# Kernel tuning notes

Measured on AMD Instinct MI355X. Metric: run time of the kernel, lower is better.

The kernel has to match this reference:

```python
import jax, jax.numpy as jnp
import numpy as np

BATCH = 131072
NUM_OSC = 4
NUM_SPEC = 300
FREQ_LO, FREQ_HI = 0.5, 5.0


def setup_inputs() -> dict:
    key = jax.random.key(0)
    ks = jax.random.split(key, 8)
    return {
        "G": jax.random.normal(ks[0], (BATCH, 8), dtype=jnp.float32),
        "W1": jax.random.normal(ks[1], (100, 8), dtype=jnp.float32) * 0.3,
        "b1": jax.random.normal(ks[2], (100,), dtype=jnp.float32) * 0.1,
        "W2": jax.random.normal(ks[3], (100, 100), dtype=jnp.float32) * 0.1,
        "b2": jax.random.normal(ks[4], (100,), dtype=jnp.float32) * 0.1,
        "W_w0": jax.random.normal(ks[5], (NUM_OSC, 100), dtype=jnp.float32) * 0.1,
        "W_wp": jax.random.normal(ks[6], (NUM_OSC, 100), dtype=jnp.float32) * 0.1,
        # torch.nn.init.uniform_(lin_g.weight, a=0.0, b=0.1)
        "W_g": jax.random.uniform(ks[7], (NUM_OSC, 100), dtype=jnp.float32) * 0.1,
    }


def reference(G, W1, b1, W2, b2, W_w0, W_wp, W_g):
    # MLP trunk: 8 -> 100 -> 100, ReLU on both layers
    out = jax.nn.relu(G @ W1.T + b1)
    out = jax.nn.relu(out @ W2.T + b2)          # (B, 100)

    # Oscillator parameter heads (bias-free), ReLU-clamped, shape (B, 4, 1)
    w0 = jax.nn.relu(out @ W_w0.T)[:, :, None]
    wp = jax.nn.relu(out @ W_wp.T)[:, :, None]
    g = jax.nn.relu(out @ W_g.T)[:, :, None]

    # Frequency grid (300,) broadcast against (B, 4, 1)
    w = jnp.arange(FREQ_LO, FREQ_HI, (FREQ_HI - FREQ_LO) / NUM_SPEC, dtype=jnp.float32)

    # Lorentz oscillator imaginary permittivity
    num = (wp ** 2) * (w * g)                   # (B, 4, 300)
    den = (w0 ** 2 - w ** 2) ** 2 + (w ** 2) * (g ** 2)
    e2 = num / den
    return jnp.sum(e2, axis=1)                  # (B, 300)
```

## Files before the change

kernel.cpp:

```cpp
#include <hip/hip_runtime.h>

#define BATCH 131072
#define NS    300
#define H     100
#define BLK   256
#define EPB   128
#define NQ4   (EPB * NS / 4)

#define REP25(M) M(0) M(1) M(2) M(3) M(4) M(5) M(6) M(7) M(8) M(9) M(10) M(11) \
  M(12) M(13) M(14) M(15) M(16) M(17) M(18) M(19) M(20) M(21) M(22) M(23) M(24)

__device__ __forceinline__ float qswap1(float x) {
    return __int_as_float(__builtin_amdgcn_mov_dpp(__float_as_int(x), 0xB1, 0xF, 0xF, true));
}
__device__ __forceinline__ float qswap2(float x) {
    return __int_as_float(__builtin_amdgcn_mov_dpp(__float_as_int(x), 0x4E, 0xF, 0xF, true));
}

__global__ __launch_bounds__(BLK, 2)
void lorentz_fused(const float* __restrict__ G,  const float* __restrict__ W1,
                   const float* __restrict__ b1, const float* __restrict__ W2,
                   const float* __restrict__ b2, const float* __restrict__ Ww0,
                   const float* __restrict__ Wwp, const float* __restrict__ Wg,
                   float* __restrict__ out)
{
    __shared__ float4 sW2c4[H * 4 * 7];
    __shared__ float4 sHead4[H * 4];
    __shared__ float4 sP04[EPB], sP14[EPB], sP24[EPB];
    __shared__ float  sW1[H * 8];
    __shared__ float  sB1[H], sB2[H];

    const int tid = threadIdx.x;

    {
        float* sW2cF = (float*)sW2c4;
        for (int i = tid; i < H * H; i += BLK) {
            int j = i / 100, k = i - j * 100;
            int q = k / 25, kk = k - q * 25;
            sW2cF[(j * 4 + q) * 28 + kk] = W2[i];
        }
        for (int i = tid; i < H * 8; i += BLK) sW1[i] = W1[i];
        for (int i = tid; i < H; i += BLK) { sB1[i] = b1[i]; sB2[i] = b2[i]; }
        float* sHeadF = (float*)sHead4;
        for (int i = tid; i < H * 4; i += BLK) {
            int j = i >> 2, q = i & 3;
            sHeadF[i * 4 + 0] = Ww0[q * H + j];
            sHeadF[i * 4 + 1] = Wwp[q * H + j];
            sHeadF[i * 4 + 2] = Wg [q * H + j];
            sHeadF[i * 4 + 3] = 0.f;
        }
    }
    __syncthreads();

    const int q  = tid & 3;
    const int pr = tid >> 2;
    const int e0 = blockIdx.x * EPB + pr * 2;

    const float4* g0p = (const float4*)(G + (size_t)e0 * 8);
    const float4 ga0 = g0p[0], gb0 = g0p[1];
    const float4 ga1 = g0p[2], gb1 = g0p[3];

#define H1DECL(i) float h1a_##i, h1b_##i;
    REP25(H1DECL)
#undef H1DECL
#define L1(i) { const float4* r = (const float4*)&sW1[(q * 25 + (i)) * 8];       \
        const float4 ra = r[0], rb = r[1];                                       \
        const float bb = sB1[q * 25 + (i)];                                      \
        float s0 = fmaf(ga0.x, ra.x, bb);  float s1 = ga0.y * ra.y;              \
        s0 = fmaf(ga0.z, ra.z, s0);  s1 = fmaf(ga0.w, ra.w, s1);                 \
        s0 = fmaf(gb0.x, rb.x, s0);  s1 = fmaf(gb0.y, rb.y, s1);                 \
        s0 = fmaf(gb0.z, rb.z, s0);  s1 = fmaf(gb0.w, rb.w, s1);                 \
        h1a_##i = fmaxf(s0 + s1, 0.f);                                           \
        float t0 = fmaf(ga1.x, ra.x, bb);  float t1 = ga1.y * ra.y;              \
        t0 = fmaf(ga1.z, ra.z, t0);  t1 = fmaf(ga1.w, ra.w, t1);                 \
        t0 = fmaf(gb1.x, rb.x, t0);  t1 = fmaf(gb1.y, rb.y, t1);                 \
        t0 = fmaf(gb1.z, rb.z, t0);  t1 = fmaf(gb1.w, rb.w, t1);                 \
        h1b_##i = fmaxf(t0 + t1, 0.f); }
    REP25(L1)
#undef L1

    float aw0a = 0.f, awpa = 0.f, agga = 0.f;
    float aw0b = 0.f, awpb = 0.f, aggb = 0.f;

#pragma unroll 2
    for (int j = 0; j < H; ++j) {
        const int cb = (j * 4 + q) * 7;
        const float4 c0 = sW2c4[cb + 0], c1 = sW2c4[cb + 1], c2 = sW2c4[cb + 2],
                     c3 = sW2c4[cb + 3], c4 = sW2c4[cb + 4], c5 = sW2c4[cb + 5],
                     c6 = sW2c4[cb + 6];
        const float4 hv  = sHead4[j * 4 + q];
        const float  b2j = sB2[j];

        float pa = 0.f, pb = 0.f;
#define CH(t, i0, i1, i2, i3)                                                    \
        pa = fmaf(h1a_##i0, c##t.x, pa); pb = fmaf(h1b_##i0, c##t.x, pb);        \
        pa = fmaf(h1a_##i1, c##t.y, pa); pb = fmaf(h1b_##i1, c##t.y, pb);        \
        pa = fmaf(h1a_##i2, c##t.z, pa); pb = fmaf(h1b_##i2, c##t.z, pb);        \
        pa = fmaf(h1a_##i3, c##t.w, pa); pb = fmaf(h1b_##i3, c##t.w, pb);
        CH(0, 0, 1, 2, 3)   CH(1, 4, 5, 6, 7)   CH(2, 8, 9, 10, 11)
        CH(3, 12, 13, 14, 15) CH(4, 16, 17, 18, 19) CH(5, 20, 21, 22, 23)
#undef CH
        pa = fmaf(h1a_24, c6.x, pa); pb = fmaf(h1b_24, c6.x, pb);

        float sa = pa + qswap1(pa); sa += qswap2(sa);
        float sb = pb + qswap1(pb); sb += qswap2(sb);
        const float h2a = fmaxf(sa + b2j, 0.f);
        const float h2b = fmaxf(sb + b2j, 0.f);

        aw0a = fmaf(h2a, hv.x, aw0a); awpa = fmaf(h2a, hv.y, awpa); agga = fmaf(h2a, hv.z, agga);
        aw0b = fmaf(h2b, hv.x, aw0b); awpb = fmaf(h2b, hv.y, awpb); aggb = fmaf(h2b, hv.z, aggb);
    }

    {
        float* P0 = (float*)sP04; float* P1 = (float*)sP14; float* P2 = (float*)sP24;
        const float w0a = fmaxf(aw0a, 0.f), wpa = fmaxf(awpa, 0.f), gga = fmaxf(agga, 0.f);
        const float w0b = fmaxf(aw0b, 0.f), wpb = fmaxf(awpb, 0.f), ggb = fmaxf(aggb, 0.f);
        const int ia = (pr * 2) * 4 + q, ib = (pr * 2 + 1) * 4 + q;
        P0[ia] = w0a * w0a;        P0[ib] = w0b * w0b;
        P1[ia] = gga * gga;        P1[ib] = ggb * ggb;
        P2[ia] = wpa * wpa * gga;  P2[ib] = wpb * wpb * ggb;
    }
    __syncthreads();

    float4* out4 = (float4*)out;
    const size_t base4 = (size_t)blockIdx.x * NQ4;

    for (int it = 0; it < (NQ4 + BLK - 1) / BLK; ++it) {
        const int idx4 = it * BLK + tid;
        if (idx4 < NQ4) {
            const int e  = idx4 / 75;
            const int k4 = idx4 - e * 75;
            const float4 P0 = sP04[e], P1 = sP14[e], P2 = sP24[e];
            const float kb = (float)(k4 << 2);
            float4 r; float* rp = (float*)&r;
#pragma unroll
            for (int i = 0; i < 4; ++i) {
                const float w   = 0.5f + (kb + (float)i) * 0.015f;
                const float wsq = w * w;
                const float t0 = P0.x - wsq, t1 = P0.y - wsq,
                            t2 = P0.z - wsq, t3 = P0.w - wsq;
                const float d0 = fmaf(t0, t0, wsq * P1.x);
                const float d1 = fmaf(t1, t1, wsq * P1.y);
                const float d2 = fmaf(t2, t2, wsq * P1.z);
                const float d3 = fmaf(t3, t3, wsq * P1.w);
                const float d01 = d0 * d1, d23 = d2 * d3;
                const float D   = d01 * d23;
                const float n01 = fmaf(P2.y, d0, P2.x * d1);
                const float n23 = fmaf(P2.w, d2, P2.z * d3);
                const float N   = fmaf(n01, d23, n23 * d01);
                rp[i] = w * (N * __builtin_amdgcn_rcpf(D));
            }
            out4[base4 + idx4] = r;
        }
    }
}

extern "C" void kernel_launch(void* const* d_in, const int* in_sizes, int n_in,
                              void* d_out, int out_size, void* d_ws, size_t ws_size,
                              hipStream_t stream) {
    const float* G   = (const float*)d_in[0];
    const float* W1  = (const float*)d_in[1];
    const float* b1  = (const float*)d_in[2];
    const float* W2  = (const float*)d_in[3];
    const float* b2  = (const float*)d_in[4];
    const float* Ww0 = (const float*)d_in[5];
    const float* Wwp = (const float*)d_in[6];
    const float* Wg  = (const float*)d_in[7];
    float* out = (float*)d_out;

    dim3 grid(BATCH / EPB);
    dim3 block(BLK);
    lorentz_fused<<<grid, block, 0, stream>>>(G, W1, b1, W2, b2, Ww0, Wwp, Wg, out);
}
```

Baseline: 90.90 us.

## Process four batch elements per thread quad to reuse W2 shared-memory loads

Each group of four threads now computes the MLP for four batch elements instead of two, doubling elements per block and halving the grid. Every W2/head value read from shared memory now feeds four FMAs instead of two, cutting LDS traffic and weight staging per element. The cost is roughly double the layer-1 activation registers (100 per thread), which risks spills or lower occupancy under launch_bounds(256,2). Since 256*300/4 divides evenly by the block size, the output loop drops its bounds check.

```diff
diff --git a/kernel.cpp b/kernel.cpp
--- a/kernel.cpp
+++ b/kernel.cpp
@@ -4,7 +4,7 @@
 #define NS    300
 #define H     100
 #define BLK   256
-#define EPB   128
+#define EPB   256
 #define NQ4   (EPB * NS / 4)
 
 #define REP25(M) M(0) M(1) M(2) M(3) M(4) M(5) M(6) M(7) M(8) M(9) M(10) M(11) \
@@ -53,34 +53,36 @@
     __syncthreads();
 
     const int q  = tid & 3;
-    const int pr = tid >> 2;
-    const int e0 = blockIdx.x * EPB + pr * 2;
+    const int gi = tid >> 2;
+    const int e0 = blockIdx.x * EPB + gi * 4;
 
-    const float4* g0p = (const float4*)(G + (size_t)e0 * 8);
-    const float4 ga0 = g0p[0], gb0 = g0p[1];
-    const float4 ga1 = g0p[2], gb1 = g0p[3];
+    const float4* gp = (const float4*)(G + (size_t)e0 * 8);
+    const float4 ga0 = gp[0], gb0 = gp[1];
+    const float4 ga1 = gp[2], gb1 = gp[3];
+    const float4 ga2 = gp[4], gb2 = gp[5];
+    const float4 ga3 = gp[6], gb3 = gp[7];
 
-#define H1DECL(i) float h1a_##i, h1b_##i;
+#define H1DECL(i) float h1a_##i, h1b_##i, h1c_##i, h1d_##i;
     REP25(H1DECL)
 #undef H1DECL
-#define L1(i) { const float4* r = (const float4*)&sW1[(q * 25 + (i)) * 8];       \
-        const float4 ra = r[0], rb = r[1];                                       \
-        const float bb = sB1[q * 25 + (i)];                                      \
-        float s0 = fmaf(ga0.x, ra.x, bb);  float s1 = ga0.y * ra.y;              \
-        s0 = fmaf(ga0.z, ra.z, s0);  s1 = fmaf(ga0.w, ra.w, s1);                 \
-        s0 = fmaf(gb0.x, rb.x, s0);  s1 = fmaf(gb0.y, rb.y, s1);                 \
-        s0 = fmaf(gb0.z, rb.z, s0);  s1 = fmaf(gb0.w, rb.w, s1);                 \
-        h1a_##i = fmaxf(s0 + s1, 0.f);                                           \
-        float t0 = fmaf(ga1.x, ra.x, bb);  float t1 = ga1.y * ra.y;              \
-        t0 = fmaf(ga1.z, ra.z, t0);  t1 = fmaf(ga1.w, ra.w, t1);                 \
-        t0 = fmaf(gb1.x, rb.x, t0);  t1 = fmaf(gb1.y, rb.y, t1);                 \
-        t0 = fmaf(gb1.z, rb.z, t0);  t1 = fmaf(gb1.w, rb.w, t1);                 \
-        h1b_##i = fmaxf(t0 + t1, 0.f); }
+#define L1E(dst, ga, gb)                                                        \
+        { float s0 = fmaf(ga.x, ra.x, bb);  float s1 = ga.y * ra.y;             \
+          s0 = fmaf(ga.z, ra.z, s0);  s1 = fmaf(ga.w, ra.w, s1);                \
+          s0 = fmaf(gb.x, rb.x, s0);  s1 = fmaf(gb.y, rb.y, s1);                \
+          s0 = fmaf(gb.z, rb.z, s0);  s1 = fmaf(gb.w, rb.w, s1);                \
+          dst = fmaxf(s0 + s1, 0.f); }
+#define L1(i) { const float4* r = (const float4*)&sW1[(q * 25 + (i)) * 8];      \
+        const float4 ra = r[0], rb = r[1];                                      \
+        const float bb = sB1[q * 25 + (i)];                                     \
+        L1E(h1a_##i, ga0, gb0)  L1E(h1b_##i, ga1, gb1)                          \
+        L1E(h1c_##i, ga2, gb2)  L1E(h1d_##i, ga3, gb3) }
     REP25(L1)
 #undef L1
 
     float aw0a = 0.f, awpa = 0.f, agga = 0.f;
     float aw0b = 0.f, awpb = 0.f, aggb = 0.f;
+    float aw0c = 0.f, awpc = 0.f, aggc = 0.f;
+    float aw0d = 0.f, awpd = 0.f, aggd = 0.f;
 
 #pragma unroll 2
     for (int j = 0; j < H; ++j) {
@@ -91,67 +93,74 @@
         const float4 hv  = sHead4[j * 4 + q];
         const float  b2j = sB2[j];
 
-        float pa = 0.f, pb = 0.f;
-#define CH(t, i0, i1, i2, i3)                                                    \
-        pa = fmaf(h1a_##i0, c##t.x, pa); pb = fmaf(h1b_##i0, c##t.x, pb);        \
-        pa = fmaf(h1a_##i1, c##t.y, pa); pb = fmaf(h1b_##i1, c##t.y, pb);        \
-        pa = fmaf(h1a_##i2, c##t.z, pa); pb = fmaf(h1b_##i2, c##t.z, pb);        \
-        pa = fmaf(h1a_##i3, c##t.w, pa); pb = fmaf(h1b_##i3, c##t.w, pb);
-        CH(0, 0, 1, 2, 3)   CH(1, 4, 5, 6, 7)   CH(2, 8, 9, 10, 11)
+        float pa = 0.f, pb = 0.f, pc = 0.f, pd = 0.f;
+#define CH1(w, i)                                                               \
+        pa = fmaf(h1a_##i, w, pa); pb = fmaf(h1b_##i, w, pb);                   \
+        pc = fmaf(h1c_##i, w, pc); pd = fmaf(h1d_##i, w, pd);
+#define CH(t, i0, i1, i2, i3)                                                   \
+        CH1(c##t.x, i0) CH1(c##t.y, i1) CH1(c##t.z, i2) CH1(c##t.w, i3)
+        CH(0, 0, 1, 2, 3)     CH(1, 4, 5, 6, 7)     CH(2, 8, 9, 10, 11)
         CH(3, 12, 13, 14, 15) CH(4, 16, 17, 18, 19) CH(5, 20, 21, 22, 23)
+        CH1(c6.x, 24)
 #undef CH
-        pa = fmaf(h1a_24, c6.x, pa); pb = fmaf(h1b_24, c6.x, pb);
-
+#undef CH1
         float sa = pa + qswap1(pa); sa += qswap2(sa);
         float sb = pb + qswap1(pb); sb += qswap2(sb);
+        float sc = pc + qswap1(pc); sc += qswap2(sc);
+        float sd = pd + qswap1(pd); sd += qswap2(sd);
         const float h2a = fmaxf(sa + b2j, 0.f);
         const float h2b = fmaxf(sb + b2j, 0.f);
+        const float h2c = fmaxf(sc + b2j, 0.f);
+        const float h2d = fmaxf(sd + b2j, 0.f);
 
         aw0a = fmaf(h2a, hv.x, aw0a); awpa = fmaf(h2a, hv.y, awpa); agga = fmaf(h2a, hv.z, agga);
         aw0b = fmaf(h2b, hv.x, aw0b); awpb = fmaf(h2b, hv.y, awpb); aggb = fmaf(h2b, hv.z, aggb);
+        aw0c = fmaf(h2c, hv.x, aw0c); awpc = fmaf(h2c, hv.y, awpc); aggc = fmaf(h2c, hv.z, aggc);
+        aw0d = fmaf(h2d, hv.x, aw0d); awpd = fmaf(h2d, hv.y, awpd); aggd = fmaf(h2d, hv.z, aggd);
     }
 
     {
         float* P0 = (float*)sP04; float* P1 = (float*)sP14; float* P2 = (float*)sP24;
-        const float w0a = fmaxf(aw0a, 0.f), wpa = fmaxf(awpa, 0.f), gga = fmaxf(agga, 0.f);
-        const float w0b = fmaxf(aw0b, 0.f), wpb = fmaxf(awpb, 0.f), ggb = fmaxf(aggb, 0.f);
-        const int ia = (pr * 2) * 4 + q, ib = (pr * 2 + 1) * 4 + q;
-        P0[ia] = w0a * w0a;        P0[ib] = w0b * w0b;
-        P1[ia] = gga * gga;        P1[ib] = ggb * ggb;
-        P2[ia] = wpa * wpa * gga;  P2[ib] = wpb * wpb * ggb;
+#define EMIT(aw, ap, ag, e)                                                     \
+        { const float w0 = fmaxf(aw, 0.f), wp = fmaxf(ap, 0.f), gg = fmaxf(ag, 0.f); \
+          const int ix = (gi * 4 + (e)) * 4 + q;                                \
+          P0[ix] = w0 * w0;  P1[ix] = gg * gg;  P2[ix] = wp * wp * gg; }
+        EMIT(aw0a, awpa, agga, 0)
+        EMIT(aw0b, awpb, aggb, 1)
+        EMIT(aw0c, awpc, aggc, 2)
+        EMIT(aw0d, awpd, aggd, 3)
+#undef EMIT
     }
     __syncthreads();
 
     float4* out4 = (float4*)out;
     const size_t base4 = (size_t)blockIdx.x * NQ4;
 
-    for (int it = 0; it < (NQ4 + BLK - 1) / BLK; ++it) {
+    for (int it = 0; it < NQ4 / BLK; ++it) {
         const int idx4 = it * BLK + tid;
-        if (idx4 < NQ4) {
-            const int e  = idx4 / 75;
-            const int k4 = idx4 - e * 75;
-            const float4 P0 = sP04[e], P1 = sP14[e], P2 = sP24[e];
-            const float kb = (float)(k4 << 2);
-            float4 r; float* rp = (float*)&r;
+        const int e  = idx4 / 75;
+        const int k4 = idx4 - e * 75;
+        const float4 P0 = sP04[e], P1 = sP14[e], P2 = sP24[e];
+        const float kb = (float)(k4 << 2);
+        float4 r; float* rp = (float*)&r;
 #pragma unroll
-            for (int i = 0; i < 4; ++i) {
-                const float w   = 0.5f + (kb + (float)i) * 0.015f;
-                const float wsq = w * w;
-                const float t0 = P0.x - wsq, t1 = P0.y - wsq,
-                            t2 = P0.z - wsq, t3 = P0.w - wsq;
-                const float d0 = fmaf(t0, t0, wsq * P1.x);
-                const float d1 = fmaf(t1, t1, wsq * P1.y);
-                const float d2 = fmaf(t2, t2, wsq * P1.z);
-                const float d3 = fmaf(t3, t3, wsq * P1.w);
-                const float d01 = d0 * d1, d23 = d2 * d3;
-                const float D   = d01 * d23;
-                const float n01 = fmaf(P2.y, d0, P2.x * d1);
-                const float n23 = fmaf(P2.w, d2, P2.z * d3);
-                const float N   = fmaf(n01, d23, n23 * d01);
-                rp[i] = w * (N * __builtin_amdgcn_rcpf(D));
-            }
-            out4[base4 + idx4] = r;
+        for (int i = 0; i < 4; ++i) {
+            const float w   = 0.5f + (kb + (float)i) * 0.015f;
+            const float wsq = w * w;
+            const float t0 = P0.x - wsq, t1 = P0.y - wsq,
+                        t2 = P0.z - wsq, t3 = P0.w - wsq;
+            const float d0 = fmaf(t0, t0, wsq * P1.x);
+            const float d1 = fmaf(t1, t1, wsq * P1.y);
+            const float d2 = fmaf(t2, t2, wsq * P1.z);
+            const float d3 = fmaf(t3, t3, wsq * P1.w);
+            const float d01 = d0 * d1, d23 = d2 * d3;
+            const float D   = d01 * d23;
+            const float n01 = fmaf(P2.y, d0, P2.x * d1);
+            const float n23 = fmaf(P2.w, d2, P2.z * d3);
+            const float N   = fmaf(n01, d23, n23 * d01);
+            rp[i] = w * (N * __builtin_amdgcn_rcpf(D));
         }
+        out4[base4 + idx4] = r;
     }
 }
 
```

After: 81.74 us. 1.11x faster.
